# Kernel tuning notes

Hardware: AMD Instinct MI355X
Metric: run time of the kernel (lower is better)

## Reference

```python
import jax, jax.numpy as jnp
import numpy as np

NUM_STEPS = 2  # consensus iterations


def psi3(r, edge_index, W3, b3):
    # one-layer message passing GNN: sum-aggregate neighbors, add self, linear, relu
    src, dst = edge_index[0], edge_index[1]
    agg = jnp.zeros_like(r).at[dst].add(r[src])
    return jax.nn.relu((r + agg) @ W3 + b3)


def setup_inputs() -> dict:
    key = jax.random.key(0)
    ks = jax.random.split(key, 12)
    N_total, C_in = 4096, 128   # global entity table
    N_s, N_t = 1024, 1024       # source / target graph sizes (B=1)
    E = 16384                   # edges per graph (avg degree 16)
    C1, C2 = 256, 256           # psi_1 / psi_2 output dims
    R = 32                      # psi_3 in_channels == out_channels
    s_in = 1.0 / np.sqrt(C_in)
    s_r = 1.0 / np.sqrt(R)
    inp = {}
    inp['inputs'] = jax.random.normal(ks[0], (N_total, C_in), jnp.float32)
    inp['index_n1'] = jax.random.randint(ks[1], (N_s,), 0, N_total)
    inp['index_n2'] = jax.random.randint(ks[2], (N_t,), 0, N_total)
    inp['edge_index_s'] = jax.random.randint(ks[3], (2, E), 0, N_s)
    inp['edge_index_t'] = jax.random.randint(ks[4], (2, E), 0, N_t)
    # psi_1 / psi_2: linear entity encoders
    inp['W1'] = jax.random.uniform(ks[5], (C_in, C1), jnp.float32, -s_in, s_in)
    inp['W2'] = jax.random.uniform(ks[6], (C_in, C2), jnp.float32, -s_in, s_in)
    # psi_3 weights
    inp['W3'] = jax.random.uniform(ks[7], (R, R), jnp.float32, -s_r, s_r)
    inp['b3'] = jnp.zeros((R,), jnp.float32)
    # consensus MLP: R -> R -> 1
    inp['Wm1'] = jax.random.uniform(ks[8], (R, R), jnp.float32, -s_r, s_r)
    inp['bm1'] = jnp.zeros((R,), jnp.float32)
    inp['Wm2'] = jax.random.uniform(ks[9], (R, 1), jnp.float32, -s_r, s_r)
    inp['bm2'] = jnp.zeros((1,), jnp.float32)
    # random node indicator functions r_s for each consensus step (drawn
    # with torch.randn inside the original forward; precomputed here)
    inp['rs_all'] = jax.random.normal(ks[10], (NUM_STEPS, N_s, R), jnp.float32)
    return inp


def reference(inputs, index_n1, index_n2, edge_index_s, edge_index_t,
              W1, W2, W3, b3, Wm1, bm1, Wm2, bm2, rs_all):
    time_emb = inputs @ W1  # psi_1
    rel_emb = inputs @ W2   # psi_2
    # h = cat(time, rel) per node; B=1 so masks are all-true
    h_s = jnp.concatenate([time_emb[index_n1], rel_emb[index_n1]], axis=-1)  # [N_s, C1+C2]
    h_t = jnp.concatenate([time_emb[index_n2], rel_emb[index_n2]], axis=-1)  # [N_t, C1+C2]
    S_hat = h_s @ h_t.T  # [N_s, N_t] dense similarity
    S_0 = jax.nn.softmax(S_hat, axis=-1)  # masked_softmax with full mask

    def step(S_hat, r_s):
        S = jax.nn.softmax(S_hat, axis=-1)
        r_t = S.T @ r_s                                  # [N_t, R]
        o_s = psi3(r_s, edge_index_s, W3, b3)            # [N_s, R]
        o_t = psi3(r_t, edge_index_t, W3, b3)            # [N_t, R]
        D = o_s[:, None, :] - o_t[None, :, :]            # [N_s, N_t, R]
        delta = (jax.nn.relu(D @ Wm1 + bm1) @ Wm2 + bm2)[..., 0]  # mlp(D).squeeze(-1)
        return S_hat + delta, None

    S_hat, _ = jax.lax.scan(step, S_hat, rs_all)
    S_L = jax.nn.softmax(S_hat, axis=-1)
    return S_0, S_L
```

## Files before the change

### kernel.cpp

```cpp
#include <hip/hip_runtime.h>
#include <math.h>

#define N_S   1024
#define N_T   1024
#define C_IN  128
#define E_EDG 16384
#define R     32
#define NSTEP 2

__global__ __launch_bounds__(128) void k_gram(const float* __restrict__ W1,
                                              const float* __restrict__ W2,
                                              float* __restrict__ G) {
    int a = blockIdx.x;
    int b = threadIdx.x;
    __shared__ float wa[512];
    for (int c = threadIdx.x; c < 256; c += 128) {
        wa[c]       = W1[a * 256 + c];
        wa[256 + c] = W2[a * 256 + c];
    }
    __syncthreads();
    float acc = 0.f;
    for (int c = 0; c < 256; ++c)
        acc += wa[c] * W1[b * 256 + c] + wa[256 + c] * W2[b * 256 + c];
    G[a * 128 + b] = acc;
}

__global__ __launch_bounds__(128) void k_ys(const float* __restrict__ X,
                                            const int* __restrict__ idx1,
                                            const float* __restrict__ G,
                                            float* __restrict__ Ys) {
    int i = blockIdx.x;
    int a = threadIdx.x;
    __shared__ float x[128];
    int row = idx1[i];
    x[a] = X[row * 128 + a];
    __syncthreads();
    float acc = 0.f;
#pragma unroll 8
    for (int d = 0; d < 128; ++d)
        acc += x[d] * G[d * 128 + a];
    Ys[i * 128 + a] = acc;
}

__global__ __launch_bounds__(256) void k_shat(const float* __restrict__ Ys,
                                              const float* __restrict__ X,
                                              const int* __restrict__ idx2,
                                              float* __restrict__ Shat) {
    __shared__ float As[64][132];
    __shared__ float Bs[64][132];
    const int i0 = blockIdx.y * 64, j0 = blockIdx.x * 64;
    const int t = threadIdx.x;
    for (int s = t; s < 64 * 32; s += 256) {
        int row = s >> 5, q = s & 31;
        float4 v = ((const float4*)(Ys + (size_t)(i0 + row) * 128))[q];
        *(float4*)&As[row][q * 4] = v;
    }
    for (int s = t; s < 64 * 32; s += 256) {
        int row = s >> 5, q = s & 31;
        int src = idx2[j0 + row];
        float4 v = ((const float4*)(X + (size_t)src * 128))[q];
        *(float4*)&Bs[row][q * 4] = v;
    }
    __syncthreads();
    const int r = t >> 4, c = t & 15;
    float acc[4][4] = {};
    for (int k = 0; k < 128; k += 4) {
        float4 ya[4], xb[4];
#pragma unroll
        for (int a = 0; a < 4; ++a) ya[a] = *(const float4*)&As[r + 16 * a][k];
#pragma unroll
        for (int b = 0; b < 4; ++b) xb[b] = *(const float4*)&Bs[c + 16 * b][k];
#pragma unroll
        for (int a = 0; a < 4; ++a)
#pragma unroll
            for (int b = 0; b < 4; ++b)
                acc[a][b] += ya[a].x * xb[b].x + ya[a].y * xb[b].y +
                             ya[a].z * xb[b].z + ya[a].w * xb[b].w;
    }
#pragma unroll
    for (int a = 0; a < 4; ++a)
#pragma unroll
        for (int b = 0; b < 4; ++b)
            Shat[(size_t)(i0 + r + 16 * a) * 1024 + (j0 + c + 16 * b)] = acc[a][b];
}

__global__ __launch_bounds__(256) void k_softmax(const float* __restrict__ Shat,
                                                 float* __restrict__ Sdst,
                                                 float* __restrict__ out0) {
    int i = blockIdx.x;
    int t = threadIdx.x;
    const float* row = Shat + (size_t)i * 1024;
    float x[4];
#pragma unroll
    for (int j = 0; j < 4; ++j) x[j] = row[t + 256 * j];
    __shared__ float red[256];
    float m = fmaxf(fmaxf(x[0], x[1]), fmaxf(x[2], x[3]));
    red[t] = m;
    __syncthreads();
    for (int s = 128; s > 0; s >>= 1) {
        if (t < s) red[t] = fmaxf(red[t], red[t + s]);
        __syncthreads();
    }
    float rowmax = red[0];
    __syncthreads();
    float e[4], sum = 0.f;
#pragma unroll
    for (int j = 0; j < 4; ++j) { e[j] = expf(x[j] - rowmax); sum += e[j]; }
    red[t] = sum;
    __syncthreads();
    for (int s = 128; s > 0; s >>= 1) {
        if (t < s) red[t] += red[t + s];
        __syncthreads();
    }
    float inv = 1.f / red[0];
#pragma unroll
    for (int j = 0; j < 4; ++j) {
        float v = e[j] * inv;
        Sdst[(size_t)i * 1024 + t + 256 * j] = v;
        if (out0) out0[(size_t)i * 1024 + t + 256 * j] = v;
    }
}

__global__ __launch_bounds__(256) void k_rt(const float* __restrict__ S,
                                            const float* __restrict__ rs,
                                            float* __restrict__ rt) {
    int j0 = blockIdx.x * 64;
    int i0 = blockIdx.y * 128;
    int t = threadIdx.x;
    int k = t & 31;
    int jg = t >> 5;
    __shared__ float Sl[16][68];
    __shared__ float Rl[16][36];
    float acc[8] = {};
    for (int ic = 0; ic < 128; ic += 16) {
        for (int s = t; s < 16 * 16; s += 256) {
            int row = s >> 4, q = s & 15;
            *(float4*)&Sl[row][q * 4] =
                ((const float4*)(S + (size_t)(i0 + ic + row) * 1024 + j0))[q];
        }
        for (int s = t; s < 16 * 8; s += 256) {
            int row = s >> 3, q = s & 7;
            *(float4*)&Rl[row][q * 4] =
                ((const float4*)(rs + (size_t)(i0 + ic + row) * 32))[q];
        }
        __syncthreads();
#pragma unroll
        for (int ii = 0; ii < 16; ++ii) {
            float rv = Rl[ii][k];
#pragma unroll
            for (int m = 0; m < 8; ++m)
                acc[m] += Sl[ii][jg * 8 + m] * rv;
        }
        __syncthreads();
    }
#pragma unroll
    for (int m = 0; m < 8; ++m)
        atomicAdd(&rt[(size_t)(j0 + jg * 8 + m) * 32 + k], acc[m]);
}

__global__ __launch_bounds__(256) void k_scatter(const int* __restrict__ es,
                                                 const int* __restrict__ et,
                                                 const float* __restrict__ rs,
                                                 const float* __restrict__ rt,
                                                 float* __restrict__ aggs,
                                                 float* __restrict__ aggt) {
    int gid = blockIdx.x * 256 + threadIdx.x;
    int k = gid & 31;
    int e = gid >> 5;
    if (e < E_EDG) {
        int src = es[e], dst = es[E_EDG + e];
        atomicAdd(&aggs[(size_t)dst * 32 + k], rs[(size_t)src * 32 + k]);
    } else {
        e -= E_EDG;
        int src = et[e], dst = et[E_EDG + e];
        atomicAdd(&aggt[(size_t)dst * 32 + k], rt[(size_t)src * 32 + k]);
    }
}

__global__ __launch_bounds__(256) void k_post(const float* __restrict__ rs,
                                              const float* __restrict__ rt,
                                              const float* __restrict__ aggs,
                                              const float* __restrict__ aggt,
                                              const float* __restrict__ W3,
                                              const float* __restrict__ b3,
                                              const float* __restrict__ Wm1,
                                              const float* __restrict__ bm1,
                                              float* __restrict__ P,
                                              float* __restrict__ Q) {
    __shared__ float w3[1024], wm1[1024];
    __shared__ float ul[8][33], ol[8][33];
    int t = threadIdx.x;
    for (int s = t; s < 1024; s += 256) { w3[s] = W3[s]; wm1[s] = Wm1[s]; }
    int row8 = t >> 5, k = t & 31;
    int grow = blockIdx.x * 8 + row8;
    bool is_s = grow < 1024;
    int r = is_s ? grow : grow - 1024;
    const float* rin = is_s ? rs : rt;
    const float* agg = is_s ? aggs : aggt;
    ul[row8][k] = rin[(size_t)r * 32 + k] + agg[(size_t)r * 32 + k];
    __syncthreads();
    float acc = b3[k];
#pragma unroll
    for (int m = 0; m < 32; ++m) acc += ul[row8][m] * w3[m * 32 + k];
    ol[row8][k] = fmaxf(acc, 0.f);
    __syncthreads();
    float acc2 = is_s ? bm1[k] : 0.f;
#pragma unroll
    for (int m = 0; m < 32; ++m) acc2 += ol[row8][m] * wm1[m * 32 + k];
    if (is_s) P[(size_t)r * 32 + k] = acc2;
    else      Q[(size_t)r * 32 + k] = acc2;
}

__global__ __launch_bounds__(256) void k_delta(const float* __restrict__ P,
                                               const float* __restrict__ Q,
                                               const float* __restrict__ Wm2,
                                               const float* __restrict__ bm2,
                                               float* __restrict__ Shat) {
    __shared__ float Pl[64][36], Ql[64][36];
    int t = threadIdx.x;
    int i0 = blockIdx.y * 64, j0 = blockIdx.x * 64;
    for (int s = t; s < 64 * 8; s += 256) {
        int row = s >> 3, q = s & 7;
        *(float4*)&Pl[row][q * 4] = ((const float4*)(P + (size_t)(i0 + row) * 32))[q];
        *(float4*)&Ql[row][q * 4] = ((const float4*)(Q + (size_t)(j0 + row) * 32))[q];
    }
    __syncthreads();
    int r = t >> 4, c = t & 15;
    float bv = bm2[0];
    float acc[4][4] = {};
#pragma unroll
    for (int q = 0; q < 8; ++q) {
        float4 w = ((const float4*)Wm2)[q];
        float4 pa[4], qb[4];
#pragma unroll
        for (int a = 0; a < 4; ++a) pa[a] = *(const float4*)&Pl[r + 16 * a][q * 4];
#pragma unroll
        for (int b = 0; b < 4; ++b) qb[b] = *(const float4*)&Ql[c + 16 * b][q * 4];
#pragma unroll
        for (int a = 0; a < 4; ++a)
#pragma unroll
            for (int b = 0; b < 4; ++b)
                acc[a][b] += w.x * fmaxf(pa[a].x - qb[b].x, 0.f)
                           + w.y * fmaxf(pa[a].y - qb[b].y, 0.f)
                           + w.z * fmaxf(pa[a].z - qb[b].z, 0.f)
                           + w.w * fmaxf(pa[a].w - qb[b].w, 0.f);
    }
#pragma unroll
    for (int a = 0; a < 4; ++a)
#pragma unroll
        for (int b = 0; b < 4; ++b) {
            size_t idx = (size_t)(i0 + r + 16 * a) * 1024 + (j0 + c + 16 * b);
            Shat[idx] += acc[a][b] + bv;
        }
}

extern "C" void kernel_launch(void* const* d_in, const int* in_sizes, int n_in,
                              void* d_out, int out_size, void* d_ws, size_t ws_size,
                              hipStream_t stream) {
    const float* inputs = (const float*)d_in[0];
    const int*   idx1   = (const int*)d_in[1];
    const int*   idx2   = (const int*)d_in[2];
    const int*   es     = (const int*)d_in[3];
    const int*   et     = (const int*)d_in[4];
    const float* W1     = (const float*)d_in[5];
    const float* W2     = (const float*)d_in[6];
    const float* W3     = (const float*)d_in[7];
    const float* b3     = (const float*)d_in[8];
    const float* Wm1    = (const float*)d_in[9];
    const float* bm1    = (const float*)d_in[10];
    const float* Wm2    = (const float*)d_in[11];
    const float* bm2    = (const float*)d_in[12];
    const float* rs_all = (const float*)d_in[13];
    float* out = (float*)d_out;
    float* ws  = (float*)d_ws;

    float* Shat = ws;
    float* S    = Shat + (1 << 20);
    float* Ys   = S + (1 << 20);
    float* G    = Ys + 131072;
    float* rt   = G + 16384;
    float* aggs = rt + 32768;
    float* aggt = aggs + 32768;
    float* P    = aggt + 32768;
    float* Q    = P + 32768;

    k_gram<<<128, 128, 0, stream>>>(W1, W2, G);
    k_ys<<<1024, 128, 0, stream>>>(inputs, idx1, G, Ys);
    k_shat<<<dim3(16, 16), 256, 0, stream>>>(Ys, inputs, idx2, Shat);

    for (int step = 0; step < NSTEP; ++step) {
        const float* rs = rs_all + (size_t)step * N_S * R;
        hipMemsetAsync(rt, 0, 3 * 32768 * sizeof(float), stream);
        k_softmax<<<1024, 256, 0, stream>>>(Shat, S, step == 0 ? out : nullptr);
        k_rt<<<dim3(16, 8), 256, 0, stream>>>(S, rs, rt);
        k_scatter<<<4096, 256, 0, stream>>>(es, et, rs, rt, aggs, aggt);
        k_post<<<256, 256, 0, stream>>>(rs, rt, aggs, aggt, W3, b3, Wm1, bm1, P, Q);
        k_delta<<<dim3(16, 16), 256, 0, stream>>>(P, Q, Wm2, bm2, Shat);
    }
    k_softmax<<<1024, 256, 0, stream>>>(Shat, out + (1 << 20), nullptr);
}
```

Measured before the change: 184.1 us.

## Fuse whole pipeline into one persistent cooperative kernel with grid barriers

Replaces the chain of about a dozen kernel launches and memsets with a single cooperative kernel of 256 blocks that steps through phases separated by software grid barriers. It also hoists the source-side psi3 and MLP work for both steps so it overlaps the Ys phase. The softmax now keeps only per-row max and inverse sum, and the r_t product recomputes exp on the fly instead of writing a full S matrix. Per-column r_t accumulation replaces atomics, and Q is fused into the delta kernel. The aim is to remove launch overhead and the S round-trips, at the cost of barrier spin latency and lower per-phase parallelism.

```diff
diff --git a/kernel.cpp b/kernel.cpp
--- a/kernel.cpp
+++ b/kernel.cpp
@@ -1,301 +1,371 @@
 #include <hip/hip_runtime.h>
-#include <math.h>
-
-#define N_S   1024
-#define N_T   1024
-#define C_IN  128
-#define E_EDG 16384
-#define R     32
-#define NSTEP 2
-
-__global__ __launch_bounds__(128) void k_gram(const float* __restrict__ W1,
-                                              const float* __restrict__ W2,
-                                              float* __restrict__ G) {
-    int a = blockIdx.x;
-    int b = threadIdx.x;
-    __shared__ float wa[512];
-    for (int c = threadIdx.x; c < 256; c += 128) {
-        wa[c]       = W1[a * 256 + c];
-        wa[256 + c] = W2[a * 256 + c];
-    }
+
+#define NS 1024
+#define NT 1024
+#define EE 16384
+#define RR 32
+
+__device__ __forceinline__ void gridbar(int* cnt, int* epoch) {
     __syncthreads();
-    float acc = 0.f;
-    for (int c = 0; c < 256; ++c)
-        acc += wa[c] * W1[b * 256 + c] + wa[256 + c] * W2[b * 256 + c];
-    G[a * 128 + b] = acc;
+    if (threadIdx.x == 0) {
+        __threadfence();
+        atomicAdd(cnt, 1);
+        int target = 256 * (++(*epoch));
+        while (__hip_atomic_load(cnt, __ATOMIC_RELAXED, __HIP_MEMORY_SCOPE_AGENT) < target)
+            __builtin_amdgcn_s_sleep(2);
+        __threadfence();
+    }
+    __syncthreads();
 }
 
-__global__ __launch_bounds__(128) void k_ys(const float* __restrict__ X,
-                                            const int* __restrict__ idx1,
-                                            const float* __restrict__ G,
-                                            float* __restrict__ Ys) {
-    int i = blockIdx.x;
-    int a = threadIdx.x;
-    __shared__ float x[128];
-    int row = idx1[i];
-    x[a] = X[row * 128 + a];
-    __syncthreads();
-    float acc = 0.f;
+__device__ __forceinline__ void softmax_row(const float* __restrict__ Shat,
+                                            float* __restrict__ outp,
+                                            float* __restrict__ mrow,
+                                            float* __restrict__ linv,
+                                            int r, bool wout, bool wstats) {
+    int ln = threadIdx.x & 63;
+    const float* row = Shat + (size_t)r * 1024;
+    float4 xv[4];
+#pragma unroll
+    for (int c = 0; c < 4; ++c) xv[c] = *(const float4*)&row[ln * 4 + c * 256];
+    float m = xv[0].x;
+#pragma unroll
+    for (int c = 0; c < 4; ++c)
+        m = fmaxf(m, fmaxf(fmaxf(xv[c].x, xv[c].y), fmaxf(xv[c].z, xv[c].w)));
+#pragma unroll
+    for (int off = 32; off >= 1; off >>= 1) m = fmaxf(m, __shfl_xor(m, off));
+    float s = 0.f;
+#pragma unroll
+    for (int c = 0; c < 4; ++c) {
+        xv[c].x = __expf(xv[c].x - m); xv[c].y = __expf(xv[c].y - m);
+        xv[c].z = __expf(xv[c].z - m); xv[c].w = __expf(xv[c].w - m);
+        s += xv[c].x + xv[c].y + xv[c].z + xv[c].w;
+    }
+#pragma unroll
+    for (int off = 32; off >= 1; off >>= 1) s += __shfl_xor(s, off);
+    float inv = 1.f / s;
+    if (wout) {
+        float* orow = outp + (size_t)r * 1024;
+#pragma unroll
+        for (int c = 0; c < 4; ++c) {
+            float4 v = {xv[c].x * inv, xv[c].y * inv, xv[c].z * inv, xv[c].w * inv};
+            *(float4*)&orow[ln * 4 + c * 256] = v;
+        }
+    }
+    if (wstats && ln == 0) { mrow[r] = m; linv[r] = inv; }
+}
+
+extern "C" __global__ void __launch_bounds__(256, 1)
+dgmc_fused(const float* __restrict__ X, const int* __restrict__ idx1,
+           const int* __restrict__ idx2, const int* __restrict__ es,
+           const int* __restrict__ et, const float* __restrict__ W1,
+           const float* __restrict__ W2, const float* __restrict__ W3,
+           const float* __restrict__ b3, const float* __restrict__ Wm1,
+           const float* __restrict__ bm1, const float* __restrict__ Wm2,
+           const float* __restrict__ bm2, const float* __restrict__ rs_all,
+           float* __restrict__ out, float* __restrict__ ws) {
+    const int blk = blockIdx.x, t = threadIdx.x;
+    int* cnt = (int*)ws;
+    float* G    = ws + 256;
+    float* Ys   = G + 16384;
+    float* Shat = Ys + 131072;
+    float* mrow = Shat + (1 << 20);
+    float* linv = mrow + 1024;
+    float* rt   = linv + 1024;
+    float* aggs = rt + 32768;
+    float* aggt = aggs + 65536;
+    float* Pst  = aggt + 65536;
+    int epoch = 0;
+
+    __shared__ union {
+        struct { float A[64][68]; float B[64][68]; } sh;
+        struct { float P[64][36]; float U[64][36]; float O[64][36];
+                 float w3[1024]; float wm1[1024]; } dl;
+        struct { float E[256][4]; float red[8][32][4]; } rtp;
+        struct { float x[8][128]; } ys;
+        struct { float w[2][512]; } gr;
+    } sm;
+
+    if (blk < 64) {
+        int a0 = blk * 2;
+        for (int s = t; s < 1024; s += 256) {
+            int r = s >> 9, c = s & 511;
+            sm.gr.w[r][c] = (c < 256) ? W1[(a0 + r) * 256 + c]
+                                      : W2[(a0 + r) * 256 + (c - 256)];
+        }
+        __syncthreads();
+        int al = t >> 7, b = t & 127;
+        const float4* w1b = (const float4*)(W1 + b * 256);
+        const float4* w2b = (const float4*)(W2 + b * 256);
+        float acc = 0.f;
+        for (int c4 = 0; c4 < 64; ++c4) {
+            float4 v1 = w1b[c4], v2 = w2b[c4];
+            const float* wa = &sm.gr.w[al][c4 * 4];
+            const float* wb = &sm.gr.w[al][256 + c4 * 4];
+            acc += v1.x * wa[0] + v1.y * wa[1] + v1.z * wa[2] + v1.w * wa[3]
+                 + v2.x * wb[0] + v2.y * wb[1] + v2.z * wb[2] + v2.w * wb[3];
+        }
+        G[(a0 + al) * 128 + b] = acc;
+    } else if (blk < 128) {
+        float4 z = {0.f, 0.f, 0.f, 0.f};
+        float4* dst = (float4*)aggs;
+        int base = (blk - 64) * 512 + t;
+        dst[base] = z; dst[base + 256] = z;
+    }
+    gridbar(cnt, &epoch);
+
+    if (blk < 128) {
+        int i0 = blk * 8;
+        for (int s = t; s < 1024; s += 256) {
+            int r = s >> 7, d = s & 127;
+            sm.ys.x[r][d] = X[(size_t)idx1[i0 + r] * 128 + d];
+        }
+        __syncthreads();
+        int a = t & 127, rp = t >> 7;
+        float acc0 = 0, acc1 = 0, acc2 = 0, acc3 = 0;
+        for (int d = 0; d < 128; ++d) {
+            float g = G[d * 128 + a];
+            acc0 += sm.ys.x[rp][d] * g;     acc1 += sm.ys.x[rp + 2][d] * g;
+            acc2 += sm.ys.x[rp + 4][d] * g; acc3 += sm.ys.x[rp + 6][d] * g;
+        }
+        Ys[(i0 + rp) * 128 + a] = acc0;     Ys[(i0 + rp + 2) * 128 + a] = acc1;
+        Ys[(i0 + rp + 4) * 128 + a] = acc2; Ys[(i0 + rp + 6) * 128 + a] = acc3;
+    } else {
+        int idx = blk - 128;
+        int pstep = idx >> 6;
+        int ebase = (idx & 63) * 256;
+        const float* rsq = rs_all + pstep * (NS * RR);
+        float* agg = aggs + pstep * 32768;
+        int k = t & 31, eg = t >> 5;
+        for (int p = 0; p < 32; ++p) {
+            int e = ebase + p * 8 + eg;
+            int src = es[e], d = es[EE + e];
+            atomicAdd(&agg[d * 32 + k], rsq[src * 32 + k]);
+        }
+    }
+    gridbar(cnt, &epoch);
+
+    {
+        int bx = blk & 15, by = blk >> 4;
+        int i0 = by * 64, j0 = bx * 64;
+        int r = t >> 4, c = t & 15;
+        float acc[4][4] = {};
+        for (int kh = 0; kh < 2; ++kh) {
+            for (int s = t; s < 64 * 16; s += 256) {
+                int row = s >> 4, q = s & 15;
+                *(float4*)&sm.sh.A[row][q * 4] =
+                    ((const float4*)(Ys + (size_t)(i0 + row) * 128 + kh * 64))[q];
+            }
+            for (int s = t; s < 64 * 16; s += 256) {
+                int row = s >> 4, q = s & 15;
+                int src = idx2[j0 + row];
+                *(float4*)&sm.sh.B[row][q * 4] =
+                    ((const float4*)(X + (size_t)src * 128 + kh * 64))[q];
+            }
+            __syncthreads();
+            for (int k = 0; k < 64; k += 4) {
+                float4 ya[4], xb[4];
+#pragma unroll
+                for (int a = 0; a < 4; ++a) ya[a] = *(const float4*)&sm.sh.A[r + 16 * a][k];
+#pragma unroll
+                for (int b = 0; b < 4; ++b) xb[b] = *(const float4*)&sm.sh.B[c + 16 * b][k];
+#pragma unroll
+                for (int a = 0; a < 4; ++a)
+#pragma unroll
+                    for (int b = 0; b < 4; ++b)
+                        acc[a][b] += ya[a].x * xb[b].x + ya[a].y * xb[b].y +
+                                     ya[a].z * xb[b].z + ya[a].w * xb[b].w;
+            }
+            __syncthreads();
+        }
+#pragma unroll
+        for (int a = 0; a < 4; ++a)
+#pragma unroll
+            for (int b = 0; b < 4; ++b)
+                Shat[(size_t)(i0 + r + 16 * a) * 1024 + (j0 + c + 16 * b)] = acc[a][b];
+    }
+    gridbar(cnt, &epoch);
+
+    for (int step = 0; step < 2; ++step) {
+        const float* rsp = rs_all + step * (NS * RR);
+        float* aggtp = aggt + step * 32768;
+        const float* Pd = Pst + step * 32768;
+
+        if (blk < 128) {
+            int wv = t >> 6;
+            softmax_row(Shat, out, mrow, linv, blk * 8 + wv,     step == 0, true);
+            softmax_row(Shat, out, mrow, linv, blk * 8 + wv + 4, step == 0, true);
+        } else if (step == 0) {
+            int idx = blk - 128;
+            int pstep = idx >> 6;
+            int r0 = (idx & 63) * 16;
+            const float* rsq = rs_all + pstep * (NS * RR);
+            const float* agq = aggs + pstep * 32768;
+            float* Pq = Pst + pstep * 32768;
+            for (int s = t; s < 1024; s += 256) { sm.dl.w3[s] = W3[s]; sm.dl.wm1[s] = Wm1[s]; }
+            int row8 = t >> 5, k = t & 31;
+            float b3k = b3[k], bm1k = bm1[k];
+            for (int pass = 0; pass < 2; ++pass) {
+                int r = r0 + pass * 8 + row8;
+                sm.dl.U[row8][k] = rsq[r * 32 + k] + agq[r * 32 + k];
+                __syncthreads();
+                float a1 = b3k;
+#pragma unroll
+                for (int m = 0; m < 32; ++m) a1 += sm.dl.U[row8][m] * sm.dl.w3[m * 32 + k];
+                sm.dl.O[row8][k] = fmaxf(a1, 0.f);
+                __syncthreads();
+                float a2 = bm1k;
+#pragma unroll
+                for (int m = 0; m < 32; ++m) a2 += sm.dl.O[row8][m] * sm.dl.wm1[m * 32 + k];
+                Pq[r * 32 + k] = a2;
+                __syncthreads();
+            }
+        }
+        gridbar(cnt, &epoch);
+
+        {
+            int j0 = blk * 4;
+            int k = t & 31, g = t >> 5;
+            float a0 = 0, a1 = 0, a2 = 0, a3 = 0;
+            for (int ci = 0; ci < 4; ++ci) {
+                int i = ci * 256 + t;
+                float4 sv = *(const float4*)(Shat + (size_t)i * 1024 + j0);
+                float mm = mrow[i], il = linv[i];
+                float4 ev;
+                ev.x = __expf(sv.x - mm) * il; ev.y = __expf(sv.y - mm) * il;
+                ev.z = __expf(sv.z - mm) * il; ev.w = __expf(sv.w - mm) * il;
+                *(float4*)&sm.rtp.E[t][0] = ev;
+                __syncthreads();
+                const float* rbase = rsp + (size_t)(ci * 256) * 32;
 #pragma unroll 8
-    for (int d = 0; d < 128; ++d)
-        acc += x[d] * G[d * 128 + a];
-    Ys[i * 128 + a] = acc;
-}
-
-__global__ __launch_bounds__(256) void k_shat(const float* __restrict__ Ys,
-                                              const float* __restrict__ X,
-                                              const int* __restrict__ idx2,
-                                              float* __restrict__ Shat) {
-    __shared__ float As[64][132];
-    __shared__ float Bs[64][132];
-    const int i0 = blockIdx.y * 64, j0 = blockIdx.x * 64;
-    const int t = threadIdx.x;
-    for (int s = t; s < 64 * 32; s += 256) {
-        int row = s >> 5, q = s & 31;
-        float4 v = ((const float4*)(Ys + (size_t)(i0 + row) * 128))[q];
-        *(float4*)&As[row][q * 4] = v;
-    }
-    for (int s = t; s < 64 * 32; s += 256) {
-        int row = s >> 5, q = s & 31;
-        int src = idx2[j0 + row];
-        float4 v = ((const float4*)(X + (size_t)src * 128))[q];
-        *(float4*)&Bs[row][q * 4] = v;
-    }
-    __syncthreads();
-    const int r = t >> 4, c = t & 15;
-    float acc[4][4] = {};
-    for (int k = 0; k < 128; k += 4) {
-        float4 ya[4], xb[4];
-#pragma unroll
-        for (int a = 0; a < 4; ++a) ya[a] = *(const float4*)&As[r + 16 * a][k];
-#pragma unroll
-        for (int b = 0; b < 4; ++b) xb[b] = *(const float4*)&Bs[c + 16 * b][k];
-#pragma unroll
-        for (int a = 0; a < 4; ++a)
-#pragma unroll
-            for (int b = 0; b < 4; ++b)
-                acc[a][b] += ya[a].x * xb[b].x + ya[a].y * xb[b].y +
-                             ya[a].z * xb[b].z + ya[a].w * xb[b].w;
-    }
-#pragma unroll
-    for (int a = 0; a < 4; ++a)
-#pragma unroll
-        for (int b = 0; b < 4; ++b)
-            Shat[(size_t)(i0 + r + 16 * a) * 1024 + (j0 + c + 16 * b)] = acc[a][b];
-}
-
-__global__ __launch_bounds__(256) void k_softmax(const float* __restrict__ Shat,
-                                                 float* __restrict__ Sdst,
-                                                 float* __restrict__ out0) {
-    int i = blockIdx.x;
-    int t = threadIdx.x;
-    const float* row = Shat + (size_t)i * 1024;
-    float x[4];
-#pragma unroll
-    for (int j = 0; j < 4; ++j) x[j] = row[t + 256 * j];
-    __shared__ float red[256];
-    float m = fmaxf(fmaxf(x[0], x[1]), fmaxf(x[2], x[3]));
-    red[t] = m;
-    __syncthreads();
-    for (int s = 128; s > 0; s >>= 1) {
-        if (t < s) red[t] = fmaxf(red[t], red[t + s]);
-        __syncthreads();
-    }
-    float rowmax = red[0];
-    __syncthreads();
-    float e[4], sum = 0.f;
-#pragma unroll
-    for (int j = 0; j < 4; ++j) { e[j] = expf(x[j] - rowmax); sum += e[j]; }
-    red[t] = sum;
-    __syncthreads();
-    for (int s = 128; s > 0; s >>= 1) {
-        if (t < s) red[t] += red[t + s];
-        __syncthreads();
-    }
-    float inv = 1.f / red[0];
-#pragma unroll
-    for (int j = 0; j < 4; ++j) {
-        float v = e[j] * inv;
-        Sdst[(size_t)i * 1024 + t + 256 * j] = v;
-        if (out0) out0[(size_t)i * 1024 + t + 256 * j] = v;
-    }
-}
-
-__global__ __launch_bounds__(256) void k_rt(const float* __restrict__ S,
-                                            const float* __restrict__ rs,
-                                            float* __restrict__ rt) {
-    int j0 = blockIdx.x * 64;
-    int i0 = blockIdx.y * 128;
-    int t = threadIdx.x;
-    int k = t & 31;
-    int jg = t >> 5;
-    __shared__ float Sl[16][68];
-    __shared__ float Rl[16][36];
-    float acc[8] = {};
-    for (int ic = 0; ic < 128; ic += 16) {
-        for (int s = t; s < 16 * 16; s += 256) {
-            int row = s >> 4, q = s & 15;
-            *(float4*)&Sl[row][q * 4] =
-                ((const float4*)(S + (size_t)(i0 + ic + row) * 1024 + j0))[q];
-        }
-        for (int s = t; s < 16 * 8; s += 256) {
-            int row = s >> 3, q = s & 7;
-            *(float4*)&Rl[row][q * 4] =
-                ((const float4*)(rs + (size_t)(i0 + ic + row) * 32))[q];
-        }
-        __syncthreads();
-#pragma unroll
-        for (int ii = 0; ii < 16; ++ii) {
-            float rv = Rl[ii][k];
-#pragma unroll
-            for (int m = 0; m < 8; ++m)
-                acc[m] += Sl[ii][jg * 8 + m] * rv;
-        }
-        __syncthreads();
-    }
-#pragma unroll
-    for (int m = 0; m < 8; ++m)
-        atomicAdd(&rt[(size_t)(j0 + jg * 8 + m) * 32 + k], acc[m]);
-}
-
-__global__ __launch_bounds__(256) void k_scatter(const int* __restrict__ es,
-                                                 const int* __restrict__ et,
-                                                 const float* __restrict__ rs,
-                                                 const float* __restrict__ rt,
-                                                 float* __restrict__ aggs,
-                                                 float* __restrict__ aggt) {
-    int gid = blockIdx.x * 256 + threadIdx.x;
-    int k = gid & 31;
-    int e = gid >> 5;
-    if (e < E_EDG) {
-        int src = es[e], dst = es[E_EDG + e];
-        atomicAdd(&aggs[(size_t)dst * 32 + k], rs[(size_t)src * 32 + k]);
-    } else {
-        e -= E_EDG;
-        int src = et[e], dst = et[E_EDG + e];
-        atomicAdd(&aggt[(size_t)dst * 32 + k], rt[(size_t)src * 32 + k]);
-    }
-}
-
-__global__ __launch_bounds__(256) void k_post(const float* __restrict__ rs,
-                                              const float* __restrict__ rt,
-                                              const float* __restrict__ aggs,
-                                              const float* __restrict__ aggt,
-                                              const float* __restrict__ W3,
-                                              const float* __restrict__ b3,
-                                              const float* __restrict__ Wm1,
-                                              const float* __restrict__ bm1,
-                                              float* __restrict__ P,
-                                              float* __restrict__ Q) {
-    __shared__ float w3[1024], wm1[1024];
-    __shared__ float ul[8][33], ol[8][33];
-    int t = threadIdx.x;
-    for (int s = t; s < 1024; s += 256) { w3[s] = W3[s]; wm1[s] = Wm1[s]; }
-    int row8 = t >> 5, k = t & 31;
-    int grow = blockIdx.x * 8 + row8;
-    bool is_s = grow < 1024;
-    int r = is_s ? grow : grow - 1024;
-    const float* rin = is_s ? rs : rt;
-    const float* agg = is_s ? aggs : aggt;
-    ul[row8][k] = rin[(size_t)r * 32 + k] + agg[(size_t)r * 32 + k];
-    __syncthreads();
-    float acc = b3[k];
-#pragma unroll
-    for (int m = 0; m < 32; ++m) acc += ul[row8][m] * w3[m * 32 + k];
-    ol[row8][k] = fmaxf(acc, 0.f);
-    __syncthreads();
-    float acc2 = is_s ? bm1[k] : 0.f;
-#pragma unroll
-    for (int m = 0; m < 32; ++m) acc2 += ol[row8][m] * wm1[m * 32 + k];
-    if (is_s) P[(size_t)r * 32 + k] = acc2;
-    else      Q[(size_t)r * 32 + k] = acc2;
-}
-
-__global__ __launch_bounds__(256) void k_delta(const float* __restrict__ P,
-                                               const float* __restrict__ Q,
-                                               const float* __restrict__ Wm2,
-                                               const float* __restrict__ bm2,
-                                               float* __restrict__ Shat) {
-    __shared__ float Pl[64][36], Ql[64][36];
-    int t = threadIdx.x;
-    int i0 = blockIdx.y * 64, j0 = blockIdx.x * 64;
-    for (int s = t; s < 64 * 8; s += 256) {
-        int row = s >> 3, q = s & 7;
-        *(float4*)&Pl[row][q * 4] = ((const float4*)(P + (size_t)(i0 + row) * 32))[q];
-        *(float4*)&Ql[row][q * 4] = ((const float4*)(Q + (size_t)(j0 + row) * 32))[q];
-    }
-    __syncthreads();
-    int r = t >> 4, c = t & 15;
-    float bv = bm2[0];
-    float acc[4][4] = {};
-#pragma unroll
-    for (int q = 0; q < 8; ++q) {
-        float4 w = ((const float4*)Wm2)[q];
-        float4 pa[4], qb[4];
-#pragma unroll
-        for (int a = 0; a < 4; ++a) pa[a] = *(const float4*)&Pl[r + 16 * a][q * 4];
-#pragma unroll
-        for (int b = 0; b < 4; ++b) qb[b] = *(const float4*)&Ql[c + 16 * b][q * 4];
-#pragma unroll
-        for (int a = 0; a < 4; ++a)
-#pragma unroll
-            for (int b = 0; b < 4; ++b)
-                acc[a][b] += w.x * fmaxf(pa[a].x - qb[b].x, 0.f)
-                           + w.y * fmaxf(pa[a].y - qb[b].y, 0.f)
-                           + w.z * fmaxf(pa[a].z - qb[b].z, 0.f)
-                           + w.w * fmaxf(pa[a].w - qb[b].w, 0.f);
-    }
-#pragma unroll
-    for (int a = 0; a < 4; ++a)
-#pragma unroll
-        for (int b = 0; b < 4; ++b) {
-            size_t idx = (size_t)(i0 + r + 16 * a) * 1024 + (j0 + c + 16 * b);
-            Shat[idx] += acc[a][b] + bv;
-        }
+                for (int ii = g * 32; ii < g * 32 + 32; ++ii) {
+                    float rv = rbase[ii * 32 + k];
+                    float4 e4 = *(const float4*)&sm.rtp.E[ii][0];
+                    a0 += e4.x * rv; a1 += e4.y * rv; a2 += e4.z * rv; a3 += e4.w * rv;
+                }
+                __syncthreads();
+            }
+            float4 av = {a0, a1, a2, a3};
+            *(float4*)&sm.rtp.red[g][k][0] = av;
+            __syncthreads();
+            if (t < 128) {
+                int j = t >> 5, kk = t & 31;
+                float s = 0.f;
+#pragma unroll
+                for (int g2 = 0; g2 < 8; ++g2) s += sm.rtp.red[g2][kk][j];
+                rt[(j0 + j) * 32 + kk] = s;
+            }
+        }
+        gridbar(cnt, &epoch);
+
+        {
+            int ebase = blk * 64;
+            int k = t & 31, eg = t >> 5;
+#pragma unroll
+            for (int p = 0; p < 8; ++p) {
+                int e = ebase + p * 8 + eg;
+                int src = et[e], d = et[EE + e];
+                atomicAdd(&aggtp[d * 32 + k], rt[src * 32 + k]);
+            }
+        }
+        gridbar(cnt, &epoch);
+
+        {
+            int bx = blk & 15, by = blk >> 4;
+            int i0 = by * 64, j0 = bx * 64;
+            for (int s = t; s < 1024; s += 256) { sm.dl.w3[s] = W3[s]; sm.dl.wm1[s] = Wm1[s]; }
+            int row8 = t >> 5, k = t & 31;
+#pragma unroll
+            for (int p = 0; p < 8; ++p) {
+                int j = p * 8 + row8;
+                sm.dl.U[j][k] = rt[(j0 + j) * 32 + k] + aggtp[(j0 + j) * 32 + k];
+                sm.dl.P[j][k] = Pd[(i0 + j) * 32 + k];
+            }
+            __syncthreads();
+            float b3k = b3[k];
+#pragma unroll
+            for (int p = 0; p < 8; ++p) {
+                int j = p * 8 + row8;
+                float a1 = b3k;
+#pragma unroll
+                for (int m = 0; m < 32; ++m) a1 += sm.dl.U[j][m] * sm.dl.w3[m * 32 + k];
+                sm.dl.O[j][k] = fmaxf(a1, 0.f);
+            }
+            __syncthreads();
+#pragma unroll
+            for (int p = 0; p < 8; ++p) {
+                int j = p * 8 + row8;
+                float a2 = 0.f;
+#pragma unroll
+                for (int m = 0; m < 32; ++m) a2 += sm.dl.O[j][m] * sm.dl.wm1[m * 32 + k];
+                sm.dl.U[j][k] = a2;
+            }
+            __syncthreads();
+            int r = t >> 4, c = t & 15;
+            float bv = bm2[0];
+            float acc[4][4] = {};
+#pragma unroll
+            for (int q = 0; q < 8; ++q) {
+                float4 w = ((const float4*)Wm2)[q];
+                float4 pa[4], qb[4];
+#pragma unroll
+                for (int a = 0; a < 4; ++a) pa[a] = *(const float4*)&sm.dl.P[r + 16 * a][q * 4];
+#pragma unroll
+                for (int b = 0; b < 4; ++b) qb[b] = *(const float4*)&sm.dl.U[c + 16 * b][q * 4];
+#pragma unroll
+                for (int a = 0; a < 4; ++a)
+#pragma unroll
+                    for (int b = 0; b < 4; ++b)
+                        acc[a][b] += w.x * fmaxf(pa[a].x - qb[b].x, 0.f)
+                                   + w.y * fmaxf(pa[a].y - qb[b].y, 0.f)
+                                   + w.z * fmaxf(pa[a].z - qb[b].z, 0.f)
+                                   + w.w * fmaxf(pa[a].w - qb[b].w, 0.f);
+            }
+#pragma unroll
+            for (int a = 0; a < 4; ++a)
+#pragma unroll
+                for (int b = 0; b < 4; ++b) {
+                    size_t id = (size_t)(i0 + r + 16 * a) * 1024 + (j0 + c + 16 * b);
+                    Shat[id] += acc[a][b] + bv;
+                }
+        }
+        gridbar(cnt, &epoch);
+    }
+
+    {
+        int wv = t >> 6;
+        softmax_row(Shat, out + (1 << 20), mrow, linv, blk * 4 + wv, true, false);
+    }
 }
 
 extern "C" void kernel_launch(void* const* d_in, const int* in_sizes, int n_in,
                               void* d_out, int out_size, void* d_ws, size_t ws_size,
                               hipStream_t stream) {
-    const float* inputs = (const float*)d_in[0];
-    const int*   idx1   = (const int*)d_in[1];
-    const int*   idx2   = (const int*)d_in[2];
-    const int*   es     = (const int*)d_in[3];
-    const int*   et     = (const int*)d_in[4];
-    const float* W1     = (const float*)d_in[5];
-    const float* W2     = (const float*)d_in[6];
-    const float* W3     = (const float*)d_in[7];
-    const float* b3     = (const float*)d_in[8];
-    const float* Wm1    = (const float*)d_in[9];
-    const float* bm1    = (const float*)d_in[10];
-    const float* Wm2    = (const float*)d_in[11];
-    const float* bm2    = (const float*)d_in[12];
-    const float* rs_all = (const float*)d_in[13];
+    const float* X   = (const float*)d_in[0];
+    const int* idx1  = (const int*)d_in[1];
+    const int* idx2  = (const int*)d_in[2];
+    const int* es    = (const int*)d_in[3];
+    const int* et    = (const int*)d_in[4];
+    const float* W1  = (const float*)d_in[5];
+    const float* W2  = (const float*)d_in[6];
+    const float* W3  = (const float*)d_in[7];
+    const float* b3  = (const float*)d_in[8];
+    const float* Wm1 = (const float*)d_in[9];
+    const float* bm1 = (const float*)d_in[10];
+    const float* Wm2 = (const float*)d_in[11];
+    const float* bm2 = (const float*)d_in[12];
+    const float* rs  = (const float*)d_in[13];
     float* out = (float*)d_out;
     float* ws  = (float*)d_ws;
 
-    float* Shat = ws;
-    float* S    = Shat + (1 << 20);
-    float* Ys   = S + (1 << 20);
-    float* G    = Ys + 131072;
-    float* rt   = G + 16384;
-    float* aggs = rt + 32768;
-    float* aggt = aggs + 32768;
-    float* P    = aggt + 32768;
-    float* Q    = P + 32768;
-
-    k_gram<<<128, 128, 0, stream>>>(W1, W2, G);
-    k_ys<<<1024, 128, 0, stream>>>(inputs, idx1, G, Ys);
-    k_shat<<<dim3(16, 16), 256, 0, stream>>>(Ys, inputs, idx2, Shat);
-
-    for (int step = 0; step < NSTEP; ++step) {
-        const float* rs = rs_all + (size_t)step * N_S * R;
-        hipMemsetAsync(rt, 0, 3 * 32768 * sizeof(float), stream);
-        k_softmax<<<1024, 256, 0, stream>>>(Shat, S, step == 0 ? out : nullptr);
-        k_rt<<<dim3(16, 8), 256, 0, stream>>>(S, rs, rt);
-        k_scatter<<<4096, 256, 0, stream>>>(es, et, rs, rt, aggs, aggt);
-        k_post<<<256, 256, 0, stream>>>(rs, rt, aggs, aggt, W3, b3, Wm1, bm1, P, Q);
-        k_delta<<<dim3(16, 16), 256, 0, stream>>>(P, Q, Wm2, bm2, Shat);
-    }
-    k_softmax<<<1024, 256, 0, stream>>>(Shat, out + (1 << 20), nullptr);
+    hipMemsetAsync(d_ws, 0, 256, stream);
+
+    void* args[] = {&X, &idx1, &idx2, &es, &et, &W1, &W2, &W3, &b3,
+                    &Wm1, &bm1, &Wm2, &bm2, &rs, &out, &ws};
+    hipError_t err = hipLaunchCooperativeKernel((const void*)dgmc_fused, dim3(256),
+                                                dim3(256), args, 0, stream);
+    if (err != hipSuccess) {
+        dgmc_fused<<<dim3(256), dim3(256), 0, stream>>>(
+            X, idx1, idx2, es, et, W1, W2, W3, b3, Wm1, bm1, Wm2, bm2, rs, out, ws);
+    }
 }
```

Measured after the change: 518.5 us. +181.7%, slower.
